# Kernel tuning notes

Measured on AMD Instinct MI355X. Metric: run time of the kernel, lower is better.

The kernel has to match this reference:

```python
import jax, jax.numpy as jnp
import numpy as np
import math

B, S, D = 8, 2048, 1024
DK = D // 2


def setup_inputs() -> dict:
    key = jax.random.key(0)
    ks = jax.random.split(key, 7)
    scale = 0.02
    return {
        "x": jax.random.normal(ks[0], (B, S, D), dtype=jnp.float32),
        "Wq": jax.random.normal(ks[1], (D, DK), dtype=jnp.float32) * scale,
        "bq": jax.random.normal(ks[2], (DK,), dtype=jnp.float32) * scale,
        "Wk": jax.random.normal(ks[3], (D, DK), dtype=jnp.float32) * scale,
        "bk": jax.random.normal(ks[4], (DK,), dtype=jnp.float32) * scale,
        "Wv": jax.random.normal(ks[5], (D, DK), dtype=jnp.float32) * scale,
        "bv": jax.random.normal(ks[6], (DK,), dtype=jnp.float32) * scale,
    }


def reference(x, Wq, bq, Wk, bk, Wv, bv):
    # QKV projections: [B,S,D] @ [D,DK] -> [B,S,DK]
    q = jnp.einsum("bsd,dk->bsk", x, Wq) + bq
    k = jnp.einsum("bsd,dk->bsk", x, Wk) + bk
    v = jnp.einsum("bsd,dk->bsk", x, Wv) + bv
    # scores: [B,S,S], scaled by sqrt(size_kernel) (NOT sqrt(d_k)) per original
    scores = jnp.einsum("bqk,bsk->bqs", q, k) / jnp.float32(math.sqrt(D))
    # softmax over dim=1 (query axis) — faithful to the original's non-standard axis
    att = jax.nn.softmax(scores, axis=1)
    # PV matmul: [B,S,S] @ [B,S,DK] -> [B,S,DK]
    out = jnp.einsum("bqs,bsk->bqk", att, v)
    # mean pool over sequence dim -> [B, DK]
    return jnp.mean(out, axis=1)
```

## Files before the change

kernel.cpp:

```cpp
#include <hip/hip_runtime.h>

#define Bb 8
#define Ss 2048
#define Dd 1024
#define DKk 512
#define CC 128
#define RPC (Ss / CC)

__global__ __launch_bounds__(256) void colsum_partial(
    const float* __restrict__ x, const float* __restrict__ bv,
    float* __restrict__ ws, float* __restrict__ out) {
    const int bid = blockIdx.x;
    const int b   = bid >> 7;
    const int c   = bid & (CC - 1);
    const int t   = threadIdx.x;
    const float4* xb = (const float4*)(x + ((size_t)b * Ss + (size_t)c * RPC) * Dd);
    float4 acc = make_float4(0.f, 0.f, 0.f, 0.f);
#pragma unroll
    for (int s = 0; s < RPC; ++s) {
        float4 v = xb[(size_t)s * (Dd / 4) + t];
        acc.x += v.x; acc.y += v.y; acc.z += v.z; acc.w += v.w;
    }
    ((float4*)(ws + ((size_t)b * CC + c) * Dd))[t] = acc;
    if (c == 0) {
        out[b * DKk + t]       = bv[t];
        out[b * DKk + t + 256] = bv[t + 256];
    }
}

__global__ __launch_bounds__(256) void gemv_acc(
    const float* __restrict__ ws, const float* __restrict__ Wv,
    float* __restrict__ out) {
    __shared__ float xb[128];
    const int seg = blockIdx.x & 7;
    const int b   = blockIdx.x >> 3;
    const int t   = threadIdx.x;
    if (t < 128) {
        const int d = seg * 128 + t;
        float s = 0.f;
#pragma unroll 8
        for (int c = 0; c < CC; ++c)
            s += ws[((size_t)b * CC + c) * Dd + d];
        xb[t] = s * (1.0f / Ss);
    }
    __syncthreads();
    const float* wv = Wv + (size_t)(seg * 128) * DKk;
    float a0 = 0.f, a1 = 0.f;
#pragma unroll 8
    for (int d = 0; d < 128; ++d) {
        const float xv = xb[d];
        a0 += xv * wv[(size_t)d * DKk + t];
        a1 += xv * wv[(size_t)d * DKk + t + 256];
    }
    atomicAdd(&out[b * DKk + t],       a0);
    atomicAdd(&out[b * DKk + t + 256], a1);
}

extern "C" void kernel_launch(void* const* d_in, const int* in_sizes, int n_in,
                              void* d_out, int out_size, void* d_ws, size_t ws_size,
                              hipStream_t stream) {
    const float* x  = (const float*)d_in[0];
    const float* Wv = (const float*)d_in[5];
    const float* bv = (const float*)d_in[6];
    float* out = (float*)d_out;
    float* ws  = (float*)d_ws;

    colsum_partial<<<dim3(Bb * CC), 256, 0, stream>>>(x, bv, ws, out);
    gemv_acc<<<dim3(64), 256, 0, stream>>>(ws, Wv, out);
}
```

Baseline: 113.2 us.

## Fuse column-sum and GEMV into one cooperative kernel with grid sync

Merges the partial column-sum pass and the GEMV accumulation into a single cooperative kernel separated by a grid-wide barrier, removing the second kernel launch and the gap between launches. It also splits the GEMV phase into 16 segments per batch instead of 8, so more blocks share that work. The cost is a grid-wide synchronization and a requirement that all 1024 blocks be co-resident, which the launch bounds are set to allow.

```diff
diff --git a/kernel.cpp b/kernel.cpp
--- a/kernel.cpp
+++ b/kernel.cpp
@@ -1,4 +1,7 @@
 #include <hip/hip_runtime.h>
+#include <hip/hip_cooperative_groups.h>
+
+namespace cg = cooperative_groups;
 
 #define Bb 8
 #define Ss 2048
@@ -6,37 +9,41 @@
 #define DKk 512
 #define CC 128
 #define RPC (Ss / CC)
+#define SEGS 16
+#define SEGD (Dd / SEGS)
 
-__global__ __launch_bounds__(256) void colsum_partial(
-    const float* __restrict__ x, const float* __restrict__ bv,
-    float* __restrict__ ws, float* __restrict__ out) {
+__global__ __launch_bounds__(256, 4) void fused_attn_collapse(
+    const float* __restrict__ x, const float* __restrict__ Wv,
+    const float* __restrict__ bv, float* __restrict__ ws,
+    float* __restrict__ out) {
     const int bid = blockIdx.x;
-    const int b   = bid >> 7;
-    const int c   = bid & (CC - 1);
     const int t   = threadIdx.x;
-    const float4* xb = (const float4*)(x + ((size_t)b * Ss + (size_t)c * RPC) * Dd);
-    float4 acc = make_float4(0.f, 0.f, 0.f, 0.f);
+
+    {
+        const int b = bid >> 7;
+        const int c = bid & (CC - 1);
+        const float4* xb = (const float4*)(x + ((size_t)b * Ss + (size_t)c * RPC) * Dd);
+        float4 acc = make_float4(0.f, 0.f, 0.f, 0.f);
 #pragma unroll
-    for (int s = 0; s < RPC; ++s) {
-        float4 v = xb[(size_t)s * (Dd / 4) + t];
-        acc.x += v.x; acc.y += v.y; acc.z += v.z; acc.w += v.w;
+        for (int s = 0; s < RPC; ++s) {
+            float4 v = xb[(size_t)s * (Dd / 4) + t];
+            acc.x += v.x; acc.y += v.y; acc.z += v.z; acc.w += v.w;
+        }
+        ((float4*)(ws + ((size_t)b * CC + c) * Dd))[t] = acc;
+        if (c == 0) {
+            out[b * DKk + t]       = bv[t];
+            out[b * DKk + t + 256] = bv[t + 256];
+        }
     }
-    ((float4*)(ws + ((size_t)b * CC + c) * Dd))[t] = acc;
-    if (c == 0) {
-        out[b * DKk + t]       = bv[t];
-        out[b * DKk + t + 256] = bv[t + 256];
-    }
-}
+    __threadfence();
+    cg::this_grid().sync();
+    if (bid >= SEGS * Bb) return;
 
-__global__ __launch_bounds__(256) void gemv_acc(
-    const float* __restrict__ ws, const float* __restrict__ Wv,
-    float* __restrict__ out) {
-    __shared__ float xb[128];
-    const int seg = blockIdx.x & 7;
-    const int b   = blockIdx.x >> 3;
-    const int t   = threadIdx.x;
-    if (t < 128) {
-        const int d = seg * 128 + t;
+    __shared__ float xb[SEGD];
+    const int seg = bid & (SEGS - 1);
+    const int b   = bid >> 4;
+    if (t < SEGD) {
+        const int d = seg * SEGD + t;
         float s = 0.f;
 #pragma unroll 8
         for (int c = 0; c < CC; ++c)
@@ -44,10 +51,10 @@
         xb[t] = s * (1.0f / Ss);
     }
     __syncthreads();
-    const float* wv = Wv + (size_t)(seg * 128) * DKk;
+    const float* wv = Wv + (size_t)(seg * SEGD) * DKk;
     float a0 = 0.f, a1 = 0.f;
 #pragma unroll 8
-    for (int d = 0; d < 128; ++d) {
+    for (int d = 0; d < SEGD; ++d) {
         const float xv = xb[d];
         a0 += xv * wv[(size_t)d * DKk + t];
         a1 += xv * wv[(size_t)d * DKk + t + 256];
@@ -65,6 +72,7 @@
     float* out = (float*)d_out;
     float* ws  = (float*)d_ws;
 
-    colsum_partial<<<dim3(Bb * CC), 256, 0, stream>>>(x, bv, ws, out);
-    gemv_acc<<<dim3(64), 256, 0, stream>>>(ws, Wv, out);
+    void* args[] = {(void*)&x, (void*)&Wv, (void*)&bv, (void*)&ws, (void*)&out};
+    hipLaunchCooperativeKernel((const void*)fused_attn_collapse,
+                               dim3(Bb * CC), dim3(256), args, 0, stream);
 }
```

Result: slower. 337.8 us (+198.4%).
